# Kernel optimization log

Measured on AMD Instinct MI355X. Metric: run time of the kernel, lower is better.

## Reference

```python
import jax, jax.numpy as jnp
import numpy as np

B, N = 128, 196
HDIM, VDIM, ATT = 512, 2048, 512


def setup_inputs() -> dict:
    key = jax.random.key(0)
    ks = jax.random.split(key, 8)
    s_w = 1.0 / np.sqrt(HDIM)
    s_u = 1.0 / np.sqrt(VDIM)
    s_v = 1.0 / np.sqrt(ATT)
    return {
        "h": jax.random.normal(ks[0], (B, HDIM), dtype=jnp.float32),
        "V": jax.random.normal(ks[1], (B, N, VDIM), dtype=jnp.float32),
        "Ww": jax.random.uniform(ks[2], (HDIM, ATT), jnp.float32, -s_w, s_w),
        "Wb": jax.random.uniform(ks[3], (ATT,), jnp.float32, -s_w, s_w),
        "Uw": jax.random.uniform(ks[4], (VDIM, ATT), jnp.float32, -s_u, s_u),
        "Ub": jax.random.uniform(ks[5], (ATT,), jnp.float32, -s_u, s_u),
        "vw": jax.random.uniform(ks[6], (ATT, 1), jnp.float32, -s_v, s_v),
        "vb": jax.random.uniform(ks[7], (1,), jnp.float32, -s_v, s_v),
    }


def reference(h, V, Ww, Wb, Uw, Ub, vw, vb):
    # W(h): [B, A]; U(V): [B, N, A]
    wh = h @ Ww + Wb
    uv = jnp.einsum("bnv,va->bna", V, Uw) + Ub
    # e: [B, N, 1] scores via v(tanh(...))
    e = jnp.tanh(wh[:, None, :] + uv) @ vw + vb
    a = jax.nn.softmax(e, axis=1)          # softmax over N locations
    ctx = jnp.sum(a * V, axis=1)            # [B, vdim]
    return ctx, a.squeeze(-1)
```

## Files before the change

### kernel.cpp

```cpp
#include <hip/hip_runtime.h>
#include <hip/hip_bf16.h>

#define B_    128
#define N_    196
#define HDIM  512
#define VDIM  2048
#define ATT   512
#define M_TOT (B_ * N_)

#define BKK 64
#define NT  (VDIM / BKK)
#define BM1 128
#define BN1 128
#define N8     ((B_ * N_ * VDIM) / 8)
#define NCONVB 12544

typedef float  f32x4  __attribute__((ext_vector_type(4)));
typedef __bf16 bf16x8 __attribute__((ext_vector_type(8)));
typedef __bf16 bf16x4 __attribute__((ext_vector_type(4)));

__device__ __forceinline__ void gload_lds16(const void* g, void* l) {
    __builtin_amdgcn_global_load_lds(
        (const __attribute__((address_space(1))) void*)g,
        (__attribute__((address_space(3))) void*)l, 16, 0, 0);
}

__device__ __forceinline__ float fast_tanh(float x) {
    float ax = fabsf(x);
    float e  = __expf(-2.f * ax);
    float t  = (1.f - e) / (1.f + e);
    return copysignf(t, x);
}

__global__ void k_convprep(const float* __restrict__ V, __bf16* __restrict__ Vb,
                           const float* __restrict__ Uw, __bf16* __restrict__ UwT,
                           const float* __restrict__ h, const float* __restrict__ Ww,
                           const float* __restrict__ Wb, const float* __restrict__ Ub,
                           float* __restrict__ whp) {
    int t = threadIdx.x;
    if (blockIdx.x < 128) {
        __shared__ float hs[HDIM];
        int b = blockIdx.x;
        hs[t]       = h[(size_t)b * HDIM + t];
        hs[t + 256] = h[(size_t)b * HDIM + t + 256];
        __syncthreads();
        float a0[8] = {0,0,0,0,0,0,0,0}, a1[8] = {0,0,0,0,0,0,0,0};
        for (int k0 = 0; k0 < HDIM; k0 += 8) {
#pragma unroll
            for (int u = 0; u < 8; ++u) {
                float hv = hs[k0 + u];
                a0[u] += hv * Ww[(size_t)(k0 + u) * ATT + t];
                a1[u] += hv * Ww[(size_t)(k0 + u) * ATT + t + 256];
            }
        }
        float s0 = ((a0[0] + a0[1]) + (a0[2] + a0[3])) + ((a0[4] + a0[5]) + (a0[6] + a0[7]));
        float s1 = ((a1[0] + a1[1]) + (a1[2] + a1[3])) + ((a1[4] + a1[5]) + (a1[6] + a1[7]));
        whp[(size_t)b * ATT + t]       = s0 + Wb[t] + Ub[t];
        whp[(size_t)b * ATT + t + 256] = s1 + Wb[t + 256] + Ub[t + 256];
    } else if (blockIdx.x < 384) {
        __shared__ __bf16 st[64][65];
        int bb = blockIdx.x - 128;
        int k0 = (bb & 31) * 64;
        int c0 = (bb >> 5) * 64;
#pragma unroll
        for (int i = 0; i < 16; ++i) {
            int lin = i * 256 + t;
            int kk = lin >> 6, cc = lin & 63;
            st[kk][cc] = (__bf16)Uw[(size_t)(k0 + kk) * ATT + c0 + cc];
        }
        __syncthreads();
#pragma unroll
        for (int i = 0; i < 16; ++i) {
            int lin = i * 256 + t;
            int cc = lin >> 6, kk = lin & 63;
            UwT[(size_t)(c0 + cc) * VDIM + k0 + kk] = st[kk][cc];
        }
    } else {
        size_t base = (size_t)(blockIdx.x - 384) * 256 + t;
        const float4* Vp = reinterpret_cast<const float4*>(V);
        float4 xs[2], ys[2];
#pragma unroll
        for (int u = 0; u < 2; ++u) {
            size_t i = base + (size_t)u * ((size_t)NCONVB * 256);
            xs[u] = Vp[2 * i];
            ys[u] = Vp[2 * i + 1];
        }
#pragma unroll
        for (int u = 0; u < 2; ++u) {
            size_t i = base + (size_t)u * ((size_t)NCONVB * 256);
            float4 x = xs[u], y = ys[u];
            bf16x8 w;
            w[0] = (__bf16)x.x; w[1] = (__bf16)x.y; w[2] = (__bf16)x.z; w[3] = (__bf16)x.w;
            w[4] = (__bf16)y.x; w[5] = (__bf16)y.y; w[6] = (__bf16)y.z; w[7] = (__bf16)y.w;
            reinterpret_cast<bf16x8*>(Vb)[i] = w;
        }
    }
}

__global__ __launch_bounds__(256, 2) void k_scores128(
    const __bf16* __restrict__ Vb, const __bf16* __restrict__ UwT,
    const float* __restrict__ whp, const float* __restrict__ vw,
    float* __restrict__ e_part)
{
    __shared__ __align__(16) __bf16 As[2][BM1][BKK];
    __shared__ __align__(16) __bf16 Bs[2][BN1][BKK];
    __shared__ float red[2][BM1];

    int bid = blockIdx.x;
    int lid = (bid & 7) * (784 / 8) + (bid >> 3);
    int mtile = lid >> 2;
    int cc    = lid & 3;
    int m0 = mtile * BM1;
    int c0 = cc * BN1;
    int t    = threadIdx.x;
    int lane = t & 63;
    int wave = t >> 6;
    int wr = wave >> 1;
    int wc = wave & 1;

    f32x4 acc[4][4];
#pragma unroll
    for (int i = 0; i < 4; ++i)
#pragma unroll
        for (int j = 0; j < 4; ++j) acc[i][j] = (f32x4){0.f, 0.f, 0.f, 0.f};

    int lr  = lane >> 3;
    int csw = ((lane & 7) ^ lr) * 8;
    const __bf16* AgS = Vb  + (size_t)(m0 + wave * 32 + lr) * VDIM + csw;
    const __bf16* BgS = UwT + (size_t)(c0 + wave * 32 + lr) * VDIM + csw;
    __bf16* Al0 = &As[0][wave * 32 + lr][(lane & 7) * 8];
    __bf16* Bl0 = &Bs[0][wave * 32 + lr][(lane & 7) * 8];

#define STAGE(buf, kt)                                                          \
    do {                                                                        \
        _Pragma("unroll")                                                       \
        for (int i = 0; i < 4; ++i) {                                           \
            gload_lds16(AgS + (kt) * BKK + (size_t)i * 8 * VDIM,                \
                        Al0 + (buf) * (BM1 * BKK) + i * 8 * BKK);               \
            gload_lds16(BgS + (kt) * BKK + (size_t)i * 8 * VDIM,                \
                        Bl0 + (buf) * (BN1 * BKK) + i * 8 * BKK);               \
        }                                                                       \
    } while (0)

    int lcol = lane & 15;
    int lg4  = lane >> 4;
    int arow0 = wr * 64;
    int bcol0 = wc * 64;

    STAGE(0, 0);
    __builtin_amdgcn_sched_barrier(0);
    STAGE(1, 1);

    for (int kt = 0; kt < NT; ++kt) {
        int buf = kt & 1;
        if (kt < NT - 1) {
            asm volatile("s_waitcnt vmcnt(8)\n\ts_barrier" ::: "memory");
        } else {
            asm volatile("s_waitcnt vmcnt(0)\n\ts_barrier" ::: "memory");
        }
        __builtin_amdgcn_sched_barrier(0);

#pragma unroll
        for (int ks = 0; ks < 2; ++ks) {
            bf16x8 af[4], bfr[4];
#pragma unroll
            for (int i = 0; i < 4; ++i) {
                int row = arow0 + i * 16 + lcol;
                int ch  = ((ks * 4 + lg4) ^ (row & 7)) * 8;
                af[i] = *reinterpret_cast<const bf16x8*>(&As[buf][row][ch]);
            }
#pragma unroll
            for (int j = 0; j < 4; ++j) {
                int row = bcol0 + j * 16 + lcol;
                int ch  = ((ks * 4 + lg4) ^ (row & 7)) * 8;
                bfr[j] = *reinterpret_cast<const bf16x8*>(&Bs[buf][row][ch]);
            }
            __builtin_amdgcn_s_setprio(1);
#pragma unroll
            for (int i = 0; i < 4; ++i)
#pragma unroll
                for (int j = 0; j < 4; ++j)
                    acc[i][j] = __builtin_amdgcn_mfma_f32_16x16x32_bf16(af[i], bfr[j], acc[i][j], 0, 0, 0);
            __builtin_amdgcn_s_setprio(0);
        }

        __builtin_amdgcn_sched_barrier(0);
        asm volatile("s_barrier" ::: "memory");
        if (kt + 2 < NT) STAGE(buf, kt + 2);
    }
#undef STAGE

    int lrow4 = lg4 * 4;
#pragma unroll
    for (int i = 0; i < 4; ++i) {
        float rs[4] = {0.f, 0.f, 0.f, 0.f};
#pragma unroll
        for (int j = 0; j < 4; ++j) {
            int col = c0 + wc * 64 + j * 16 + lcol;
            float vwv = vw[col];
#pragma unroll
            for (int r = 0; r < 4; ++r) {
                int m = m0 + wr * 64 + i * 16 + lrow4 + r;
                int b = m / N_;
                float x = acc[i][j][r] + whp[(size_t)b * ATT + col];
                rs[r] += fast_tanh(x) * vwv;
            }
        }
#pragma unroll
        for (int r = 0; r < 4; ++r) {
            float v = rs[r];
            v += __shfl_xor(v, 1);
            v += __shfl_xor(v, 2);
            v += __shfl_xor(v, 4);
            v += __shfl_xor(v, 8);
            if (lcol == 0)
                red[wc][wr * 64 + i * 16 + lrow4 + r] = v;
        }
    }
    __syncthreads();
    if (t < BM1)
        e_part[(size_t)cc * M_TOT + m0 + t] = red[0][t] + red[1][t];
}

__global__ __launch_bounds__(256, 2) void k_scores_small(
    const float* __restrict__ Vf, const __bf16* __restrict__ UwT,
    const float* __restrict__ whp, const float* __restrict__ vw,
    float* __restrict__ e_part)
{
    __shared__ __align__(16) __bf16 As[2][BM1][BKK];
    __shared__ __align__(16) __bf16 Bs[2][BN1][BKK];
    __shared__ float red[2][BM1];

    int bid = blockIdx.x;
    int lid = (bid & 7) * (784 / 8) + (bid >> 3);
    int mtile = lid >> 2;
    int cc    = lid & 3;
    int m0 = mtile * BM1;
    int c0 = cc * BN1;
    int t    = threadIdx.x;
    int lane = t & 63;
    int wave = t >> 6;
    int wr = wave >> 1;
    int wc = wave & 1;

    f32x4 acc[4][4];
#pragma unroll
    for (int i = 0; i < 4; ++i)
#pragma unroll
        for (int j = 0; j < 4; ++j) acc[i][j] = (f32x4){0.f, 0.f, 0.f, 0.f};

    int lr  = lane >> 3;
    int csw = ((lane & 7) ^ lr) * 8;
    const __bf16* BgS = UwT + (size_t)(c0 + wave * 32 + lr) * VDIM + csw;
    __bf16* Bl0 = &Bs[0][wave * 32 + lr][(lane & 7) * 8];

    int ra = t >> 1;
    int ka = (t & 1) * 32;
    const float* Af = Vf + (size_t)(m0 + ra) * VDIM + ka;

#define STAGE1(buf, kt)                                                         \
    do {                                                                        \
        _Pragma("unroll")                                                       \
        for (int i = 0; i < 4; ++i)                                             \
            gload_lds16(BgS + (kt) * BKK + (size_t)i * 8 * VDIM,                \
                        Bl0 + (buf) * (BN1 * BKK) + i * 8 * BKK);               \
        const float4* src = reinterpret_cast<const float4*>(Af + (kt) * BKK);   \
        _Pragma("unroll")                                                       \
        for (int i = 0; i < 4; ++i) {                                           \
            float4 x = src[2 * i];                                              \
            float4 y = src[2 * i + 1];                                          \
            bf16x8 w;                                                           \
            w[0] = (__bf16)x.x; w[1] = (__bf16)x.y;                             \
            w[2] = (__bf16)x.z; w[3] = (__bf16)x.w;                             \
            w[4] = (__bf16)y.x; w[5] = (__bf16)y.y;                             \
            w[6] = (__bf16)y.z; w[7] = (__bf16)y.w;                             \
            int ch = (((t & 1) * 4 + i) ^ (ra & 7)) * 8;                        \
            *reinterpret_cast<bf16x8*>(&As[buf][ra][ch]) = w;                   \
        }                                                                       \
    } while (0)

    int lcol = lane & 15;
    int lg4  = lane >> 4;
    int arow0 = wr * 64;
    int bcol0 = wc * 64;

    STAGE1(0, 0);
    __syncthreads();

    for (int kt = 0; kt < NT; ++kt) {
        int buf = kt & 1;
        if (kt + 1 < NT) STAGE1(buf ^ 1, kt + 1);
#pragma unroll
        for (int ks = 0; ks < 2; ++ks) {
            bf16x8 af[4], bfr[4];
#pragma unroll
            for (int i = 0; i < 4; ++i) {
                int row = arow0 + i * 16 + lcol;
                int ch  = ((ks * 4 + lg4) ^ (row & 7)) * 8;
                af[i] = *reinterpret_cast<const bf16x8*>(&As[buf][row][ch]);
            }
#pragma unroll
            for (int j = 0; j < 4; ++j) {
                int row = bcol0 + j * 16 + lcol;
                int ch  = ((ks * 4 + lg4) ^ (row & 7)) * 8;
                bfr[j] = *reinterpret_cast<const bf16x8*>(&Bs[buf][row][ch]);
            }
#pragma unroll
            for (int i = 0; i < 4; ++i)
#pragma unroll
                for (int j = 0; j < 4; ++j)
                    acc[i][j] = __builtin_amdgcn_mfma_f32_16x16x32_bf16(af[i], bfr[j], acc[i][j], 0, 0, 0);
        }
        __syncthreads();
    }
#undef STAGE1

    int lrow4 = lg4 * 4;
#pragma unroll
    for (int i = 0; i < 4; ++i) {
        float rs[4] = {0.f, 0.f, 0.f, 0.f};
#pragma unroll
        for (int j = 0; j < 4; ++j) {
            int col = c0 + wc * 64 + j * 16 + lcol;
            float vwv = vw[col];
#pragma unroll
            for (int r = 0; r < 4; ++r) {
                int m = m0 + wr * 64 + i * 16 + lrow4 + r;
                int b = m / N_;
                float x = acc[i][j][r] + whp[(size_t)b * ATT + col];
                rs[r] += fast_tanh(x) * vwv;
            }
        }
#pragma unroll
        for (int r = 0; r < 4; ++r) {
            float v = rs[r];
            v += __shfl_xor(v, 1);
            v += __shfl_xor(v, 2);
            v += __shfl_xor(v, 4);
            v += __shfl_xor(v, 8);
            if (lcol == 0)
                red[wc][wr * 64 + i * 16 + lrow4 + r] = v;
        }
    }
    __syncthreads();
    if (t < BM1)
        e_part[(size_t)cc * M_TOT + m0 + t] = red[0][t] + red[1][t];
}

__global__ void k_ctx_sm(const __bf16* __restrict__ Vb, const float* __restrict__ e_part,
                         const float* __restrict__ vb, float* __restrict__ a_out,
                         float* __restrict__ ctx) {
    int b  = blockIdx.x;
    int ch = blockIdx.y;
    int t  = threadIdx.x;
    __shared__ float sm[256];
    __shared__ float as_[N_];

    float ev = 0.f;
    float e  = -1e30f;
    if (t < N_) {
        int m = b * N_ + t;
        ev = e_part[m] + e_part[M_TOT + m] + e_part[2 * M_TOT + m] + e_part[3 * M_TOT + m] + vb[0];
        e = ev;
    }
    sm[t] = e;
    __syncthreads();
    for (int s = 128; s > 0; s >>= 1) {
        if (t < s) sm[t] = fmaxf(sm[t], sm[t + s]);
        __syncthreads();
    }
    float mx = sm[0];
    __syncthreads();
    float ex = (t < N_) ? __expf(ev - mx) : 0.f;
    sm[t] = ex;
    __syncthreads();
    for (int s = 128; s > 0; s >>= 1) {
        if (t < s) sm[t] += sm[t + s];
        __syncthreads();
    }
    float inv = 1.f / sm[0];
    if (t < N_) {
        as_[t] = ex * inv;
        if (ch == 0) a_out[(size_t)b * N_ + t] = ex * inv;
    }
    __syncthreads();

    int col = ch * 1024 + t * 4;
    const __bf16* Vp = Vb + (size_t)b * N_ * VDIM + col;
    float av[4] = {0.f, 0.f, 0.f, 0.f};
    for (int n = 0; n < N_; ++n) {
        bf16x4 v = *reinterpret_cast<const bf16x4*>(Vp + (size_t)n * VDIM);
        float an = as_[n];
#pragma unroll
        for (int j = 0; j < 4; ++j) av[j] += an * (float)v[j];
    }
    f32x4 o = {av[0], av[1], av[2], av[3]};
    *reinterpret_cast<f32x4*>(ctx + (size_t)b * VDIM + col) = o;
}

__global__ void k_softmax(const float* __restrict__ e_part, const float* __restrict__ vb,
                          float* __restrict__ a_out) {
    int b = blockIdx.x;
    int t = threadIdx.x;
    __shared__ float sm[256];
    float ev = 0.f;
    float e  = -1e30f;
    if (t < N_) {
        int m = b * N_ + t;
        ev = e_part[m] + e_part[M_TOT + m] + e_part[2 * M_TOT + m] + e_part[3 * M_TOT + m] + vb[0];
        e = ev;
    }
    sm[t] = e;
    __syncthreads();
    for (int s = 128; s > 0; s >>= 1) {
        if (t < s) sm[t] = fmaxf(sm[t], sm[t + s]);
        __syncthreads();
    }
    float mx = sm[0];
    __syncthreads();
    float ex = (t < N_) ? __expf(ev - mx) : 0.f;
    sm[t] = ex;
    __syncthreads();
    for (int s = 128; s > 0; s >>= 1) {
        if (t < s) sm[t] += sm[t + s];
        __syncthreads();
    }
    float inv = 1.f / sm[0];
    if (t < N_) a_out[(size_t)b * N_ + t] = ex * inv;
}

__global__ void k_ctx_f32(const float* __restrict__ V, const float* __restrict__ a,
                          float* __restrict__ ctx) {
    int b  = blockIdx.x;
    int ch = blockIdx.y;
    int t  = threadIdx.x;
    __shared__ float as_[N_];
    for (int i = t; i < N_; i += 128) as_[i] = a[(size_t)b * N_ + i];
    __syncthreads();
    int col = ch * 512 + t * 4;
    const f32x4* Vp = reinterpret_cast<const f32x4*>(V + (size_t)b * N_ * VDIM + col);
    f32x4 accv = {0.f, 0.f, 0.f, 0.f};
    for (int n = 0; n < N_; ++n)
        accv += as_[n] * Vp[(size_t)n * (VDIM / 4)];
    *reinterpret_cast<f32x4*>(ctx + (size_t)b * VDIM + col) = accv;
}

extern "C" void kernel_launch(void* const* d_in, const int* in_sizes, int n_in,
                              void* d_out, int out_size, void* d_ws, size_t ws_size,
                              hipStream_t stream) {
    const float* h  = (const float*)d_in[0];
    const float* V  = (const float*)d_in[1];
    const float* Ww = (const float*)d_in[2];
    const float* Wb = (const float*)d_in[3];
    const float* Uw = (const float*)d_in[4];
    const float* Ub = (const float*)d_in[5];
    const float* vw = (const float*)d_in[6];
    const float* vb = (const float*)d_in[7];

    float* out     = (float*)d_out;
    float* ctx_out = out;
    float* a_out   = out + (size_t)B_ * VDIM;

    const size_t vb_bytes = (size_t)B_ * N_ * VDIM * sizeof(__bf16);
    const size_t tail     = 2u * 1024 * 1024 + 256 * 1024 + (size_t)4 * M_TOT * 4 + 4096;
    bool preconv = ws_size >= vb_bytes + tail;

    char*   ws   = (char*)d_ws;
    __bf16* Vb   = (__bf16*)ws;
    char*   rest = ws + (preconv ? vb_bytes : 0);
    __bf16* UwT   = (__bf16*)rest;
    float*  whp   = (float*)(rest + 2u * 1024 * 1024);
    float*  e_prt = (float*)(rest + 2u * 1024 * 1024 + 256 * 1024);

    int grid_cp = preconv ? (384 + NCONVB) : 384;
    k_convprep<<<dim3(grid_cp), 256, 0, stream>>>(
        V, Vb, Uw, UwT, h, Ww, Wb, Ub, whp);
    if (preconv) {
        k_scores128<<<dim3(784), 256, 0, stream>>>(Vb, UwT, whp, vw, e_prt);
        k_ctx_sm<<<dim3(B_, 2), 256, 0, stream>>>(Vb, e_prt, vb, a_out, ctx_out);
    } else {
        k_scores_small<<<dim3(784), 256, 0, stream>>>(V, UwT, whp, vw, e_prt);
        k_softmax<<<dim3(B_), 256, 0, stream>>>(e_prt, vb, a_out);
        k_ctx_f32<<<dim3(B_, 4), 128, 0, stream>>>(V, a_out, ctx_out);
    }
}
```

Baseline: 149.4 us.

## Enlarge scores GEMM tile to 256x256 with 512-thread blocks

Replaces the 128x128 scores GEMM tile with a 256x256 tile computed by 8 waves (each 128x64), cutting the grid from 784 to 196 blocks and the number of column partials from 4 to 2. The larger tile halves global/L2 traffic per FLOP for both V and Uw operands. The XCD remapping is adjusted for 196 blocks, and the softmax/context kernel now sums a variable number of partials. The trade-offs are higher register pressure (32 accumulators per thread), 128KB of LDS per block, and fewer blocks than CUs (196 on a 256-CU part), which may underutilize the GPU.

```diff
diff --git a/kernel.cpp b/kernel.cpp
--- a/kernel.cpp
+++ b/kernel.cpp
@@ -12,6 +12,8 @@
 #define NT  (VDIM / BKK)
 #define BM1 128
 #define BN1 128
+#define BM2 256
+#define BN2 256
 #define N8     ((B_ * N_ * VDIM) / 8)
 #define NCONVB 12544
 
@@ -97,30 +99,32 @@
     }
 }
 
-__global__ __launch_bounds__(256, 2) void k_scores128(
+__global__ __launch_bounds__(512, 2) void k_scores256(
     const __bf16* __restrict__ Vb, const __bf16* __restrict__ UwT,
     const float* __restrict__ whp, const float* __restrict__ vw,
     float* __restrict__ e_part)
 {
-    __shared__ __align__(16) __bf16 As[2][BM1][BKK];
-    __shared__ __align__(16) __bf16 Bs[2][BN1][BKK];
-    __shared__ float red[2][BM1];
+    __shared__ __align__(16) __bf16 As[2][BM2][BKK];
+    __shared__ __align__(16) __bf16 Bs[2][BN2][BKK];
+    __shared__ float red[4][BM2];
 
     int bid = blockIdx.x;
-    int lid = (bid & 7) * (784 / 8) + (bid >> 3);
-    int mtile = lid >> 2;
-    int cc    = lid & 3;
-    int m0 = mtile * BM1;
-    int c0 = cc * BN1;
+    int xcd = bid & 7, ix = bid >> 3;
+    int lid = (xcd < 4 ? xcd * 25 : 100 + (xcd - 4) * 24) + ix;
+    int mtile = lid >> 1;
+    int cc    = lid & 1;
+    int m0 = mtile * BM2;
+    int c0 = cc * BN2;
+
     int t    = threadIdx.x;
     int lane = t & 63;
     int wave = t >> 6;
-    int wr = wave >> 1;
-    int wc = wave & 1;
-
-    f32x4 acc[4][4];
-#pragma unroll
-    for (int i = 0; i < 4; ++i)
+    int wr = wave >> 2;
+    int wc = wave & 3;
+
+    f32x4 acc[8][4];
+#pragma unroll
+    for (int i = 0; i < 8; ++i)
 #pragma unroll
         for (int j = 0; j < 4; ++j) acc[i][j] = (f32x4){0.f, 0.f, 0.f, 0.f};
 
@@ -131,25 +135,25 @@
     __bf16* Al0 = &As[0][wave * 32 + lr][(lane & 7) * 8];
     __bf16* Bl0 = &Bs[0][wave * 32 + lr][(lane & 7) * 8];
 
-#define STAGE(buf, kt)                                                          \
+#define STAGE2(buf, kt)                                                         \
     do {                                                                        \
         _Pragma("unroll")                                                       \
         for (int i = 0; i < 4; ++i) {                                           \
             gload_lds16(AgS + (kt) * BKK + (size_t)i * 8 * VDIM,                \
-                        Al0 + (buf) * (BM1 * BKK) + i * 8 * BKK);               \
+                        Al0 + (buf) * (BM2 * BKK) + i * 8 * BKK);               \
             gload_lds16(BgS + (kt) * BKK + (size_t)i * 8 * VDIM,                \
-                        Bl0 + (buf) * (BN1 * BKK) + i * 8 * BKK);               \
+                        Bl0 + (buf) * (BN2 * BKK) + i * 8 * BKK);               \
         }                                                                       \
     } while (0)
 
     int lcol = lane & 15;
     int lg4  = lane >> 4;
-    int arow0 = wr * 64;
+    int arow0 = wr * 128;
     int bcol0 = wc * 64;
 
-    STAGE(0, 0);
+    STAGE2(0, 0);
     __builtin_amdgcn_sched_barrier(0);
-    STAGE(1, 1);
+    STAGE2(1, 1);
 
     for (int kt = 0; kt < NT; ++kt) {
         int buf = kt & 1;
@@ -162,22 +166,22 @@
 
 #pragma unroll
         for (int ks = 0; ks < 2; ++ks) {
-            bf16x8 af[4], bfr[4];
-#pragma unroll
-            for (int i = 0; i < 4; ++i) {
-                int row = arow0 + i * 16 + lcol;
-                int ch  = ((ks * 4 + lg4) ^ (row & 7)) * 8;
-                af[i] = *reinterpret_cast<const bf16x8*>(&As[buf][row][ch]);
-            }
+            bf16x8 bfr[4], af[8];
 #pragma unroll
             for (int j = 0; j < 4; ++j) {
                 int row = bcol0 + j * 16 + lcol;
                 int ch  = ((ks * 4 + lg4) ^ (row & 7)) * 8;
                 bfr[j] = *reinterpret_cast<const bf16x8*>(&Bs[buf][row][ch]);
             }
+#pragma unroll
+            for (int i = 0; i < 8; ++i) {
+                int row = arow0 + i * 16 + lcol;
+                int ch  = ((ks * 4 + lg4) ^ (row & 7)) * 8;
+                af[i] = *reinterpret_cast<const bf16x8*>(&As[buf][row][ch]);
+            }
             __builtin_amdgcn_s_setprio(1);
 #pragma unroll
-            for (int i = 0; i < 4; ++i)
+            for (int i = 0; i < 8; ++i)
 #pragma unroll
                 for (int j = 0; j < 4; ++j)
                     acc[i][j] = __builtin_amdgcn_mfma_f32_16x16x32_bf16(af[i], bfr[j], acc[i][j], 0, 0, 0);
@@ -186,13 +190,13 @@
 
         __builtin_amdgcn_sched_barrier(0);
         asm volatile("s_barrier" ::: "memory");
-        if (kt + 2 < NT) STAGE(buf, kt + 2);
-    }
-#undef STAGE
+        if (kt + 2 < NT) STAGE2(buf, kt + 2);
+    }
+#undef STAGE2
 
     int lrow4 = lg4 * 4;
 #pragma unroll
-    for (int i = 0; i < 4; ++i) {
+    for (int i = 0; i < 8; ++i) {
         float rs[4] = {0.f, 0.f, 0.f, 0.f};
 #pragma unroll
         for (int j = 0; j < 4; ++j) {
@@ -200,7 +204,7 @@
             float vwv = vw[col];
 #pragma unroll
             for (int r = 0; r < 4; ++r) {
-                int m = m0 + wr * 64 + i * 16 + lrow4 + r;
+                int m = m0 + wr * 128 + i * 16 + lrow4 + r;
                 int b = m / N_;
                 float x = acc[i][j][r] + whp[(size_t)b * ATT + col];
                 rs[r] += fast_tanh(x) * vwv;
@@ -214,12 +218,13 @@
             v += __shfl_xor(v, 4);
             v += __shfl_xor(v, 8);
             if (lcol == 0)
-                red[wc][wr * 64 + i * 16 + lrow4 + r] = v;
-        }
-    }
-    __syncthreads();
-    if (t < BM1)
-        e_part[(size_t)cc * M_TOT + m0 + t] = red[0][t] + red[1][t];
+                red[wc][wr * 128 + i * 16 + lrow4 + r] = v;
+        }
+    }
+    __syncthreads();
+    if (t < BM2)
+        e_part[(size_t)cc * M_TOT + m0 + t] =
+            red[0][t] + red[1][t] + red[2][t] + red[3][t];
 }
 
 __global__ __launch_bounds__(256, 2) void k_scores_small(
@@ -349,7 +354,7 @@
 
 __global__ void k_ctx_sm(const __bf16* __restrict__ Vb, const float* __restrict__ e_part,
                          const float* __restrict__ vb, float* __restrict__ a_out,
-                         float* __restrict__ ctx) {
+                         float* __restrict__ ctx, int npart) {
     int b  = blockIdx.x;
     int ch = blockIdx.y;
     int t  = threadIdx.x;
@@ -360,7 +365,8 @@
     float e  = -1e30f;
     if (t < N_) {
         int m = b * N_ + t;
-        ev = e_part[m] + e_part[M_TOT + m] + e_part[2 * M_TOT + m] + e_part[3 * M_TOT + m] + vb[0];
+        ev = vb[0];
+        for (int p = 0; p < npart; ++p) ev += e_part[(size_t)p * M_TOT + m];
         e = ev;
     }
     sm[t] = e;
@@ -476,8 +482,8 @@
     k_convprep<<<dim3(grid_cp), 256, 0, stream>>>(
         V, Vb, Uw, UwT, h, Ww, Wb, Ub, whp);
     if (preconv) {
-        k_scores128<<<dim3(784), 256, 0, stream>>>(Vb, UwT, whp, vw, e_prt);
-        k_ctx_sm<<<dim3(B_, 2), 256, 0, stream>>>(Vb, e_prt, vb, a_out, ctx_out);
+        k_scores256<<<dim3(196), 512, 0, stream>>>(Vb, UwT, whp, vw, e_prt);
+        k_ctx_sm<<<dim3(B_, 2), 256, 0, stream>>>(Vb, e_prt, vb, a_out, ctx_out, 2);
     } else {
         k_scores_small<<<dim3(784), 256, 0, stream>>>(V, UwT, whp, vw, e_prt);
         k_softmax<<<dim3(B_), 256, 0, stream>>>(e_prt, vb, a_out);
```

New measurement: 143.4 us, median of 3. 1.04x faster.
